# Optimization experiments

Measured on AMD Instinct MI355X. Metric: run time of the kernel, lower is better.

## Reference

```python
import jax, jax.numpy as jnp
import numpy as np

EMBED_DIM = 1024
NUM_HEADS = 16
HEAD_DIM = EMBED_DIM // NUM_HEADS
B, S = 2, 2048


def setup_inputs() -> dict:
    key = jax.random.key(0)
    ks = jax.random.split(key, 11)
    sc = 1.0 / np.sqrt(EMBED_DIM)
    d = {
        'query': jax.random.normal(ks[0], (B, S, EMBED_DIM), jnp.float32),
        'key': jax.random.normal(ks[1], (B, S, EMBED_DIM), jnp.float32),
        'value': jax.random.normal(ks[2], (B, S, EMBED_DIM), jnp.float32),
        'Wq': jax.random.normal(ks[3], (EMBED_DIM, EMBED_DIM), jnp.float32) * sc,
        'bq': jnp.zeros((EMBED_DIM,), jnp.float32),
        'Wk': jax.random.normal(ks[4], (EMBED_DIM, EMBED_DIM), jnp.float32) * sc,
        'bk': jnp.zeros((EMBED_DIM,), jnp.float32),
        'Wv': jax.random.normal(ks[5], (EMBED_DIM, EMBED_DIM), jnp.float32) * sc,
        'bv': jnp.zeros((EMBED_DIM,), jnp.float32),
        'Wo': jax.random.normal(ks[6], (EMBED_DIM, EMBED_DIM), jnp.float32) * sc,
        'bo': jnp.zeros((EMBED_DIM,), jnp.float32),
    }
    return d


def reference(query, key, value, Wq, bq, Wk, bk, Wv, bv, Wo, bo):
    b, s, _ = query.shape
    scale = 1.0 / np.sqrt(HEAD_DIM)
    # projections: torch Linear is x @ W.T + b
    q = (query @ Wq.T + bq).reshape(b, s, NUM_HEADS, HEAD_DIM).transpose(0, 2, 1, 3)
    k = (key @ Wk.T + bk).reshape(b, s, NUM_HEADS, HEAD_DIM).transpose(0, 2, 1, 3)
    v = (value @ Wv.T + bv).reshape(b, s, NUM_HEADS, HEAD_DIM).transpose(0, 2, 1, 3)
    scores = jnp.einsum('bhqd,bhkd->bhqk', q, k) * scale  # [B,H,S,S]
    causal = jnp.triu(jnp.ones((s, s), bool), k=1)
    scores = jnp.where(causal, -jnp.inf, scores)
    attn = jax.nn.softmax(scores, axis=-1)
    out = jnp.einsum('bhqk,bhkd->bhqd', attn, v)
    out = out.transpose(0, 2, 1, 3).reshape(b, s, EMBED_DIM)
    out = out @ Wo.T + bo
    return out, attn
```

## Files before the change

### kernel.cpp

```cpp
#include <hip/hip_runtime.h>
#include <hip/hip_bf16.h>

#define BATCH  2
#define SEQ    2048
#define EMBED  1024
#define NHEADS 16
#define HDIM   64
#define SCALE  0.125f
#define S2     0.180336880f
#define MFIX   20.0f
#define PPITCH 72

typedef __attribute__((ext_vector_type(8))) short   short8;
typedef __attribute__((ext_vector_type(4))) float   floatx4;

#if __has_builtin(__builtin_amdgcn_exp2f)
#define EXP2(x) __builtin_amdgcn_exp2f(x)
#else
#define EXP2(x) exp2f(x)
#endif

#define GLOAD_LDS(g, l) __builtin_amdgcn_global_load_lds(                      \
    (const __attribute__((address_space(1))) void*)(const void*)(g),           \
    (__attribute__((address_space(3))) void*)(void*)(l), 16, 0, 0)

__device__ __forceinline__ float bf2f(unsigned short h) {
    union { unsigned int u; float f; } v; v.u = ((unsigned int)h) << 16; return v.f;
}
__device__ __forceinline__ unsigned short f2bf(float f) {
    union { float f; unsigned int u; } v; v.f = f;
    unsigned int r = v.u + 0x7FFF + ((v.u >> 16) & 1);
    return (unsigned short)(r >> 16);
}
__device__ __forceinline__ unsigned int pack2(float lo, float hi) {
    return (unsigned int)f2bf(lo) | ((unsigned int)f2bf(hi) << 16);
}

__device__ __forceinline__ void bar_lds() {
    __builtin_amdgcn_sched_barrier(0);
    asm volatile("s_waitcnt lgkmcnt(0)" ::: "memory");
    __builtin_amdgcn_s_barrier();
    __builtin_amdgcn_sched_barrier(0);
}

__global__ __launch_bounds__(256)
void cvt_bf16(const float* __restrict__ q,  const float* __restrict__ k,
              const float* __restrict__ v,  const float* __restrict__ wq,
              const float* __restrict__ wk, const float* __restrict__ wv,
              const float* __restrict__ wo,
              unsigned short* __restrict__ dq,  unsigned short* __restrict__ dk,
              unsigned short* __restrict__ dv,  unsigned short* __restrict__ dwq,
              unsigned short* __restrict__ dwk, unsigned short* __restrict__ dwv,
              unsigned short* __restrict__ dwo)
{
    const float* s; unsigned short* d; int n;
    switch (blockIdx.y) {
        case 0: s = q;  d = dq;  n = BATCH * SEQ * EMBED; break;
        case 1: s = k;  d = dk;  n = BATCH * SEQ * EMBED; break;
        case 2: s = v;  d = dv;  n = BATCH * SEQ * EMBED; break;
        case 3: s = wq; d = dwq; n = EMBED * EMBED; break;
        case 4: s = wk; d = dwk; n = EMBED * EMBED; break;
        case 5: s = wv; d = dwv; n = EMBED * EMBED; break;
        default: s = wo; d = dwo; n = EMBED * EMBED; break;
    }
    const int i = (blockIdx.x * 256 + threadIdx.x) * 8;
    if (i >= n) return;
    float4 f0 = ((const float4*)(s + i))[0];
    float4 f1 = ((const float4*)(s + i))[1];
    uint4 u = {pack2(f0.x, f0.y), pack2(f0.z, f0.w),
               pack2(f1.x, f1.y), pack2(f1.z, f1.w)};
    *(uint4*)(d + i) = u;
}

__device__ __forceinline__ void gemm_body(
    const unsigned short* __restrict__ A,
    const unsigned short* __restrict__ W,
    const float* __restrict__ bias,
    void* __restrict__ Cout, const int f32out,
    const int bx, const int by)
{
    constexpr int N = EMBED;
    constexpr int K = EMBED;

    __shared__ unsigned short As[128 * 64];
    __shared__ unsigned short Bs[128 * 64];

    const int t    = threadIdx.x;
    const int w    = t >> 6;
    const int lane = t & 63;
    const int lr   = lane & 15;
    const int quad = lane >> 4;
    const int wr   = w >> 1;
    const int wc   = w & 1;
    const int n0   = bx * 128;
    const int m0   = by * 128;

    size_t agoff[4], bgoff[4];
    #pragma unroll
    for (int i = 0; i < 4; ++i) {
        const int slot = i * 256 + t;
        const int row  = slot >> 3;
        const int g    = (slot & 7) ^ (row & 7);
        agoff[i] = (size_t)(m0 + row) * K + g * 8;
        bgoff[i] = (size_t)(n0 + row) * K + g * 8;
    }

    int aoff[4][2], boff[4][2];
    #pragma unroll
    for (int mb = 0; mb < 4; ++mb)
        #pragma unroll
        for (int s = 0; s < 2; ++s) {
            const int row = wr * 64 + mb * 16 + lr;
            aoff[mb][s] = row * 64 + (((s * 4 + quad) ^ (row & 7)) * 8);
        }
    #pragma unroll
    for (int nb = 0; nb < 4; ++nb)
        #pragma unroll
        for (int s = 0; s < 2; ++s) {
            const int row = wc * 64 + nb * 16 + lr;
            boff[nb][s] = row * 64 + (((s * 4 + quad) ^ (row & 7)) * 8);
        }

    floatx4 acc[4][4];
    #pragma unroll
    for (int mb = 0; mb < 4; ++mb)
        #pragma unroll
        for (int nb = 0; nb < 4; ++nb) acc[mb][nb] = (floatx4){0.f, 0.f, 0.f, 0.f};

    for (int k0 = 0; k0 < K; k0 += 64) {
        __syncthreads();
        #pragma unroll
        for (int i = 0; i < 4; ++i)
            GLOAD_LDS(A + agoff[i] + k0, &As[(i * 256 + w * 64) * 8]);
        #pragma unroll
        for (int i = 0; i < 4; ++i)
            GLOAD_LDS(W + bgoff[i] + k0, &Bs[(i * 256 + w * 64) * 8]);
        __syncthreads();

        #pragma unroll
        for (int s = 0; s < 2; ++s) {
            short8 av[4], bv[4];
            #pragma unroll
            for (int mb = 0; mb < 4; ++mb) av[mb] = *(const short8*)&As[aoff[mb][s]];
            #pragma unroll
            for (int nb = 0; nb < 4; ++nb) bv[nb] = *(const short8*)&Bs[boff[nb][s]];
            #pragma unroll
            for (int mb = 0; mb < 4; ++mb)
                #pragma unroll
                for (int nb = 0; nb < 4; ++nb)
                    acc[mb][nb] = __builtin_amdgcn_mfma_f32_16x16x32_bf16(av[mb], bv[nb], acc[mb][nb], 0, 0, 0);
        }
    }

    #pragma unroll
    for (int mb = 0; mb < 4; ++mb)
        #pragma unroll
        for (int nb = 0; nb < 4; ++nb) {
            const int col = n0 + wc * 64 + nb * 16 + lr;
            const float bv = bias[col];
            #pragma unroll
            for (int r = 0; r < 4; ++r) {
                const int row = m0 + wr * 64 + mb * 16 + quad * 4 + r;
                const float val = acc[mb][nb][r] + bv;
                if (f32out) ((float*)Cout)[(size_t)row * N + col] = val;
                else        ((unsigned short*)Cout)[(size_t)row * N + col] = f2bf(val);
            }
        }
}

__global__ __launch_bounds__(256)
void gemm_qkv(const unsigned short* __restrict__ xq, const unsigned short* __restrict__ xk,
              const unsigned short* __restrict__ xv,
              const unsigned short* __restrict__ wq, const unsigned short* __restrict__ wk,
              const unsigned short* __restrict__ wv,
              const float* __restrict__ bq, const float* __restrict__ bk,
              const float* __restrict__ bv,
              unsigned short* __restrict__ Qb, unsigned short* __restrict__ Kb,
              unsigned short* __restrict__ Vb)
{
    const unsigned short *A, *W; const float* bias; unsigned short* C;
    switch (blockIdx.z) {
        case 0:  A = xq; W = wq; bias = bq; C = Qb; break;
        case 1:  A = xk; W = wk; bias = bk; C = Kb; break;
        default: A = xv; W = wv; bias = bv; C = Vb; break;
    }
    gemm_body(A, W, bias, C, 0, blockIdx.x, blockIdx.y);
}

__global__ __launch_bounds__(256)
void attn_pass(const unsigned short* __restrict__ Qb,
               const unsigned short* __restrict__ Kb,
               const unsigned short* __restrict__ Vb,
               unsigned short* __restrict__ Pb,
               float* __restrict__ Lbuf,
               unsigned short* __restrict__ AO)
{
    __shared__ unsigned short Ks[2][64][PPITCH];
    __shared__ unsigned short Vt[2][64][PPITCH];
    __shared__ unsigned short Ps[64][PPITCH];

    const int t    = threadIdx.x;
    const int w    = t >> 6;
    const int lane = t & 63;
    const int lr   = lane & 15;
    const int quad = lane >> 4;
    const int h    = blockIdx.y;
    const int b    = blockIdx.z;
    const int slot = (h >> 3) + 2 * b;
    const int qt   = (slot & 1) ? (SEQ / 64 - 1 - (int)blockIdx.x) : (int)blockIdx.x;
    const int q0   = qt * 64;
    const int srow = t >> 2;
    const int sseg = (t & 3) * 16;
    const int bh   = b * NHEADS + h;

    const size_t kvbase = (size_t)b * SEQ * EMBED + h * HDIM;

    const unsigned short* qrow = Qb + kvbase + (size_t)(q0 + w * 16 + lr) * EMBED + quad * 8;
    const short8 af0 = *(const short8*)(qrow);
    const short8 af1 = *(const short8*)(qrow + 32);

    const unsigned short* Krow = Kb + kvbase + (size_t)srow * EMBED + sseg;
    const unsigned short* Vrow = Vb + kvbase + (size_t)lane * EMBED;

    uint4 kA0, kA1, vA0, vA1;
    uint4 kB0, kB1, vB0, vB1;

    kA0 = ((const uint4*)Krow)[0];
    kA1 = ((const uint4*)Krow)[1];
    vA0 = *(const uint4*)(Vrow + w * 8);
    vA1 = *(const uint4*)(Vrow + (w + 4) * 8);
    *(uint4*)&Ks[0][srow][sseg]     = kA0;
    *(uint4*)&Ks[0][srow][sseg + 8] = kA1;
    {
        const unsigned short* p0 = (const unsigned short*)&vA0;
        const unsigned short* p1 = (const unsigned short*)&vA1;
        #pragma unroll
        for (int j = 0; j < 8; ++j) Vt[0][w * 8 + j][lane]       = p0[j];
        #pragma unroll
        for (int j = 0; j < 8; ++j) Vt[0][(w + 4) * 8 + j][lane] = p1[j];
    }
    if (qt > 0) {
        const unsigned short* kp = Krow + (size_t)64 * EMBED;
        kB0 = ((const uint4*)kp)[0];
        kB1 = ((const uint4*)kp)[1];
        vB0 = *(const uint4*)(Vrow + (size_t)64 * EMBED + w * 8);
        vB1 = *(const uint4*)(Vrow + (size_t)64 * EMBED + (w + 4) * 8);
    }
    bar_lds();

    float lsum[4];
    #pragma unroll
    for (int r = 0; r < 4; ++r) lsum[r] = 0.f;
    floatx4 of[4];
    #pragma unroll
    for (int i = 0; i < 4; ++i) of[i] = (floatx4){0.f, 0.f, 0.f, 0.f};

    unsigned short* pb_bh = Pb + (size_t)bh * SEQ * (SEQ * 2);
    const int rrow = lane >> 2;
    const int rseg = (lane & 3) * 16;

    for (int kt = 0; kt <= qt; ++kt) {
        const int c  = kt & 1;
        const int k0 = kt * 64;

        if (kt < qt) {
            if ((kt & 1) == 0) {
                *(uint4*)&Ks[c ^ 1][srow][sseg]     = kB0;
                *(uint4*)&Ks[c ^ 1][srow][sseg + 8] = kB1;
                const unsigned short* p0 = (const unsigned short*)&vB0;
                const unsigned short* p1 = (const unsigned short*)&vB1;
                #pragma unroll
                for (int j = 0; j < 8; ++j) Vt[c ^ 1][w * 8 + j][lane]       = p0[j];
                #pragma unroll
                for (int j = 0; j < 8; ++j) Vt[c ^ 1][(w + 4) * 8 + j][lane] = p1[j];
                if (kt + 2 <= qt) {
                    const unsigned short* kp = Krow + (size_t)(k0 + 128) * EMBED;
                    kA0 = ((const uint4*)kp)[0];
                    kA1 = ((const uint4*)kp)[1];
                    vA0 = *(const uint4*)(Vrow + (size_t)(k0 + 128) * EMBED + w * 8);
                    vA1 = *(const uint4*)(Vrow + (size_t)(k0 + 128) * EMBED + (w + 4) * 8);
                }
            } else {
                *(uint4*)&Ks[c ^ 1][srow][sseg]     = kA0;
                *(uint4*)&Ks[c ^ 1][srow][sseg + 8] = kA1;
                const unsigned short* p0 = (const unsigned short*)&vA0;
                const unsigned short* p1 = (const unsigned short*)&vA1;
                #pragma unroll
                for (int j = 0; j < 8; ++j) Vt[c ^ 1][w * 8 + j][lane]       = p0[j];
                #pragma unroll
                for (int j = 0; j < 8; ++j) Vt[c ^ 1][(w + 4) * 8 + j][lane] = p1[j];
                if (kt + 2 <= qt) {
                    const unsigned short* kp = Krow + (size_t)(k0 + 128) * EMBED;
                    kB0 = ((const uint4*)kp)[0];
                    kB1 = ((const uint4*)kp)[1];
                    vB0 = *(const uint4*)(Vrow + (size_t)(k0 + 128) * EMBED + w * 8);
                    vB1 = *(const uint4*)(Vrow + (size_t)(k0 + 128) * EMBED + (w + 4) * 8);
                }
            }
        }

        floatx4 sf[4];
        #pragma unroll
        for (int i = 0; i < 4; ++i) sf[i] = (floatx4){0.f, 0.f, 0.f, 0.f};
        #pragma unroll
        for (int nb = 0; nb < 4; ++nb) {
            short8 bf0 = *(const short8*)&Ks[c][nb * 16 + lr][quad * 8];
            sf[nb] = __builtin_amdgcn_mfma_f32_16x16x32_bf16(af0, bf0, sf[nb], 0, 0, 0);
        }
        #pragma unroll
        for (int nb = 0; nb < 4; ++nb) {
            short8 bf1 = *(const short8*)&Ks[c][nb * 16 + lr][32 + quad * 8];
            sf[nb] = __builtin_amdgcn_mfma_f32_16x16x32_bf16(af1, bf1, sf[nb], 0, 0, 0);
        }

        if (kt < qt) {
            #pragma unroll
            for (int nb = 0; nb < 4; ++nb)
                #pragma unroll
                for (int r = 0; r < 4; ++r) {
                    float p = EXP2(sf[nb][r] * S2 - MFIX);
                    lsum[r] += p;
                    Ps[w * 16 + quad * 4 + r][nb * 16 + lr] = f2bf(p);
                }
        } else {
            #pragma unroll
            for (int nb = 0; nb < 4; ++nb) {
                const int k = nb * 16 + lr;
                #pragma unroll
                for (int r = 0; r < 4; ++r) {
                    const int q = w * 16 + quad * 4 + r;
                    float p = 0.f;
                    if (k <= q) { p = EXP2(sf[nb][r] * S2 - MFIX); lsum[r] += p; }
                    Ps[w * 16 + quad * 4 + r][nb * 16 + lr] = f2bf(p);
                }
            }
        }

        {
            const unsigned short* ps = &Ps[w * 16 + rrow][rseg];
            unsigned short* op = pb_bh + (size_t)(q0 + w * 16 + rrow) * (SEQ * 2) + k0 + rseg;
            *(uint4*)op       = *(const uint4*)ps;
            *(uint4*)(op + 8) = *(const uint4*)(ps + 8);
        }

        #pragma unroll
        for (int ss = 0; ss < 2; ++ss) {
            short8 paf = *(const short8*)&Ps[w * 16 + lr][ss * 32 + quad * 8];
            #pragma unroll
            for (int nb = 0; nb < 4; ++nb) {
                short8 vf = *(const short8*)&Vt[c][nb * 16 + lr][ss * 32 + quad * 8];
                of[nb] = __builtin_amdgcn_mfma_f32_16x16x32_bf16(paf, vf, of[nb], 0, 0, 0);
            }
        }

        bar_lds();
    }

    float invl[4];
    #pragma unroll
    for (int r = 0; r < 4; ++r) {
        #pragma unroll
        for (int off = 1; off < 16; off <<= 1)
            lsum[r] += __shfl_xor(lsum[r], off, 64);
        invl[r] = 1.f / lsum[r];
    }
    if (lr == 0) {
        #pragma unroll
        for (int r = 0; r < 4; ++r)
            Lbuf[(size_t)bh * SEQ + q0 + w * 16 + quad * 4 + r] = invl[r];
    }

    #pragma unroll
    for (int nb = 0; nb < 4; ++nb)
        #pragma unroll
        for (int r = 0; r < 4; ++r)
            Ps[w * 16 + quad * 4 + r][nb * 16 + lr] = f2bf(of[nb][r] * invl[r]);
    {
        unsigned short* ao = AO + (size_t)(b * SEQ + q0 + w * 16 + rrow) * EMBED + h * HDIM + rseg;
        *(uint4*)ao       = *(const uint4*)&Ps[w * 16 + rrow][rseg];
        *(uint4*)(ao + 8) = *(const uint4*)&Ps[w * 16 + rrow][rseg + 8];
    }
}

__global__ __launch_bounds__(256)
void out_norm(const unsigned short* __restrict__ AO, const unsigned short* __restrict__ Wo16,
              const float* __restrict__ bo, float* __restrict__ out,
              float* __restrict__ attn, const float* __restrict__ Lbuf)
{
    const int id = blockIdx.x;
    if (id < 256) {
        gemm_body(AO, Wo16, bo, out, 1, id & 7, id >> 3);
        return;
    }
    const int id2   = id - 256;
    const int bh    = id2 >> 5;
    const int x     = id2 & 31;
    const int chunk = (bh & 1) ? (31 - x) : x;
    const int t     = threadIdx.x;
    const int w     = t >> 6;
    const int lane  = t & 63;

    const unsigned short* pb = (const unsigned short*)(attn + (size_t)bh * SEQ * SEQ);
    float* ab = attn + (size_t)bh * SEQ * SEQ;

    for (int i = 0; i < 16; ++i) {
        const int q  = chunk * 64 + w * 16 + i;
        const int qc = (q & ~63) + 64;
        const float il = Lbuf[(size_t)bh * SEQ + q];
        const unsigned short* src = pb + (size_t)q * (SEQ * 2);
        float* dst = ab + (size_t)q * SEQ;

        uint4 rr[4];
        #pragma unroll
        for (int s = 0; s < 4; ++s) {
            const int c = lane * 8 + s * 512;
            if (c < qc) rr[s] = *(const uint4*)(src + c);
        }
        #pragma unroll
        for (int s = 0; s < 4; ++s) {
            const int c = lane * 8 + s * 512;
            if (c < qc) {
                const unsigned short* u = (const unsigned short*)&rr[s];
                float4 f0 = {bf2f(u[0]) * il, bf2f(u[1]) * il, bf2f(u[2]) * il, bf2f(u[3]) * il};
                float4 f1 = {bf2f(u[4]) * il, bf2f(u[5]) * il, bf2f(u[6]) * il, bf2f(u[7]) * il};
                ((float4*)(dst + c))[0] = f0;
                ((float4*)(dst + c))[1] = f1;
            }
        }
        for (int c = qc + lane * 8; c < SEQ; c += 512) {
            float4 z = {0.f, 0.f, 0.f, 0.f};
            ((float4*)(dst + c))[0] = z;
            ((float4*)(dst + c))[1] = z;
        }
    }
}

extern "C" void kernel_launch(void* const* d_in, const int* in_sizes, int n_in,
                              void* d_out, int out_size, void* d_ws, size_t ws_size,
                              hipStream_t stream)
{
    const float* query = (const float*)d_in[0];
    const float* key   = (const float*)d_in[1];
    const float* value = (const float*)d_in[2];
    const float* Wq    = (const float*)d_in[3];
    const float* bq    = (const float*)d_in[4];
    const float* Wk    = (const float*)d_in[5];
    const float* bk    = (const float*)d_in[6];
    const float* Wv    = (const float*)d_in[7];
    const float* bv    = (const float*)d_in[8];
    const float* Wo    = (const float*)d_in[9];
    const float* bo    = (const float*)d_in[10];

    float* out  = (float*)d_out;
    float* attn = out + (size_t)BATCH * SEQ * EMBED;

    const size_t tsz = (size_t)BATCH * SEQ * EMBED;
    const size_t wsz = (size_t)EMBED * EMBED;
    unsigned short* p = (unsigned short*)d_ws;
    unsigned short* xq  = p;  p += tsz;
    unsigned short* xk  = p;  p += tsz;
    unsigned short* xv  = p;  p += tsz;
    unsigned short* wq16 = p; p += wsz;
    unsigned short* wk16 = p; p += wsz;
    unsigned short* wv16 = p; p += wsz;
    unsigned short* wo16 = p; p += wsz;
    unsigned short* Qb  = p;  p += tsz;
    unsigned short* Kb  = p;  p += tsz;
    unsigned short* Vb  = p;  p += tsz;
    unsigned short* AO  = p;  p += tsz;

    float* Lbuf = (float*)xq;

    const dim3 blk(256);

    cvt_bf16<<<dim3(2048, 7), blk, 0, stream>>>(query, key, value, Wq, Wk, Wv, Wo,
                                                xq, xk, xv, wq16, wk16, wv16, wo16);

    const dim3 gqkv(EMBED / 128, (BATCH * SEQ) / 128, 3);
    gemm_qkv<<<gqkv, blk, 0, stream>>>(xq, xk, xv, wq16, wk16, wv16,
                                       bq, bk, bv, Qb, Kb, Vb);

    attn_pass<<<dim3(SEQ / 64, NHEADS, BATCH), blk, 0, stream>>>(
        Qb, Kb, Vb, (unsigned short*)attn, Lbuf, AO);

    out_norm<<<dim3(256 + 1024), blk, 0, stream>>>(AO, wo16, bo, out, attn, Lbuf);
}
```

Baseline: 836.4 us.

## Fuse attention-probability normalization into attention kernel, split out-projection GEMM

The attention kernel now keeps the inverse row sums in shared memory and, after a full wait, re-reads its own unnormalized bf16 probability rows and writes the normalized fp32 rows plus zero padding in place. This removes the global Lbuf round trip and the separate normalization blocks that used to share a launch with the output GEMM. The output projection now runs as its own GEMM kernel. The re-read is meant to hit cache while the rows are still hot, but the normalization work is now serialized inside the attention blocks instead of overlapping with the output GEMM.

Result: faster. 808.5 us (-3.3%).

```diff
diff --git a/kernel.cpp b/kernel.cpp
--- a/kernel.cpp
+++ b/kernel.cpp
@@ -188,16 +188,23 @@
 }
 
 __global__ __launch_bounds__(256)
+void gemm_out(const unsigned short* __restrict__ A, const unsigned short* __restrict__ W,
+              const float* __restrict__ bias, float* __restrict__ Cout)
+{
+    gemm_body(A, W, bias, Cout, 1, blockIdx.x, blockIdx.y);
+}
+
+__global__ __launch_bounds__(256)
 void attn_pass(const unsigned short* __restrict__ Qb,
                const unsigned short* __restrict__ Kb,
                const unsigned short* __restrict__ Vb,
                unsigned short* __restrict__ Pb,
-               float* __restrict__ Lbuf,
                unsigned short* __restrict__ AO)
 {
     __shared__ unsigned short Ks[2][64][PPITCH];
     __shared__ unsigned short Vt[2][64][PPITCH];
     __shared__ unsigned short Ps[64][PPITCH];
+    __shared__ float          Linv[64];
 
     const int t    = threadIdx.x;
     const int w    = t >> 6;
@@ -367,7 +374,7 @@
     if (lr == 0) {
         #pragma unroll
         for (int r = 0; r < 4; ++r)
-            Lbuf[(size_t)bh * SEQ + q0 + w * 16 + quad * 4 + r] = invl[r];
+            Linv[w * 16 + quad * 4 + r] = invl[r];
     }
 
     #pragma unroll
@@ -380,57 +387,39 @@
         *(uint4*)ao       = *(const uint4*)&Ps[w * 16 + rrow][rseg];
         *(uint4*)(ao + 8) = *(const uint4*)&Ps[w * 16 + rrow][rseg + 8];
     }
-}
-
-__global__ __launch_bounds__(256)
-void out_norm(const unsigned short* __restrict__ AO, const unsigned short* __restrict__ Wo16,
-              const float* __restrict__ bo, float* __restrict__ out,
-              float* __restrict__ attn, const float* __restrict__ Lbuf)
-{
-    const int id = blockIdx.x;
-    if (id < 256) {
-        gemm_body(AO, Wo16, bo, out, 1, id & 7, id >> 3);
-        return;
-    }
-    const int id2   = id - 256;
-    const int bh    = id2 >> 5;
-    const int x     = id2 & 31;
-    const int chunk = (bh & 1) ? (31 - x) : x;
-    const int t     = threadIdx.x;
-    const int w     = t >> 6;
-    const int lane  = t & 63;
-
-    const unsigned short* pb = (const unsigned short*)(attn + (size_t)bh * SEQ * SEQ);
-    float* ab = attn + (size_t)bh * SEQ * SEQ;
-
+
+    __builtin_amdgcn_sched_barrier(0);
+    asm volatile("s_waitcnt vmcnt(0) lgkmcnt(0)" ::: "memory");
+    __builtin_amdgcn_sched_barrier(0);
+
+    float* fb = ((float*)Pb) + (size_t)bh * SEQ * SEQ;
+    const int qc = q0 + 64;
     for (int i = 0; i < 16; ++i) {
-        const int q  = chunk * 64 + w * 16 + i;
-        const int qc = (q & ~63) + 64;
-        const float il = Lbuf[(size_t)bh * SEQ + q];
-        const unsigned short* src = pb + (size_t)q * (SEQ * 2);
-        float* dst = ab + (size_t)q * SEQ;
+        const int q  = q0 + w * 16 + i;
+        const float il = Linv[w * 16 + i];
+        const unsigned short* src = pb_bh + (size_t)q * (SEQ * 2);
+        float* dst = fb + (size_t)q * SEQ;
 
         uint4 rr[4];
         #pragma unroll
         for (int s = 0; s < 4; ++s) {
-            const int c = lane * 8 + s * 512;
-            if (c < qc) rr[s] = *(const uint4*)(src + c);
+            const int cc = s * 512 + lane * 8;
+            if (cc < qc) rr[s] = *(const uint4*)(src + cc);
         }
         #pragma unroll
         for (int s = 0; s < 4; ++s) {
-            const int c = lane * 8 + s * 512;
-            if (c < qc) {
+            const int cc = s * 512 + lane * 8;
+            if (cc < qc) {
                 const unsigned short* u = (const unsigned short*)&rr[s];
                 float4 f0 = {bf2f(u[0]) * il, bf2f(u[1]) * il, bf2f(u[2]) * il, bf2f(u[3]) * il};
                 float4 f1 = {bf2f(u[4]) * il, bf2f(u[5]) * il, bf2f(u[6]) * il, bf2f(u[7]) * il};
-                ((float4*)(dst + c))[0] = f0;
-                ((float4*)(dst + c))[1] = f1;
+                ((float4*)(dst + cc))[0] = f0;
+                ((float4*)(dst + cc))[1] = f1;
+            } else {
+                float4 z = {0.f, 0.f, 0.f, 0.f};
+                ((float4*)(dst + cc))[0] = z;
+                ((float4*)(dst + cc))[1] = z;
             }
-        }
-        for (int c = qc + lane * 8; c < SEQ; c += 512) {
-            float4 z = {0.f, 0.f, 0.f, 0.f};
-            ((float4*)(dst + c))[0] = z;
-            ((float4*)(dst + c))[1] = z;
         }
     }
 }
@@ -469,8 +458,6 @@
     unsigned short* Vb  = p;  p += tsz;
     unsigned short* AO  = p;  p += tsz;
 
-    float* Lbuf = (float*)xq;
-
     const dim3 blk(256);
 
     cvt_bf16<<<dim3(2048, 7), blk, 0, stream>>>(query, key, value, Wq, Wk, Wv, Wo,
@@ -481,7 +468,7 @@
                                        bq, bk, bv, Qb, Kb, Vb);
 
     attn_pass<<<dim3(SEQ / 64, NHEADS, BATCH), blk, 0, stream>>>(
-        Qb, Kb, Vb, (unsigned short*)attn, Lbuf, AO);
-
-    out_norm<<<dim3(256 + 1024), blk, 0, stream>>>(AO, wo16, bo, out, attn, Lbuf);
-}
+        Qb, Kb, Vb, (unsigned short*)attn, AO);
+
+    gemm_out<<<dim3(EMBED / 128, (BATCH * SEQ) / 128), blk, 0, stream>>>(AO, wo16, bo, out);
+}
```
